# Optimization experiments

Measured on AMD Instinct MI355X. Metric: run time of the kernel, lower is better.

Reference implementation:

```python
import jax, jax.numpy as jnp
import numpy as np

# SPU activation from the RAI-2021 project: x^2 - 0.5 for x>=0, sigmoid(-x)-1 for x<0.

def spu(x):
    s = jax.nn.sigmoid(-x)
    return jnp.where(x >= 0, x * x - 0.5, s - 1.0)

def dspu(x):
    s = jax.nn.sigmoid(-x)
    return jnp.where(x >= 0, 2.0 * x, -s * (1.0 - s))

def get_homog(w, b):
    # [[w, b], [0, 1]]: maps coeff rows over layer outputs (out+1) -> coeffs over inputs (in+1)
    top = jnp.concatenate([w, b[:, None]], axis=1)
    bot = jnp.concatenate([jnp.zeros((1, w.shape[1]), w.dtype), jnp.ones((1, 1), w.dtype)], axis=1)
    return jnp.concatenate([top, bot], axis=0)

def slope_clip(l, u, w_l, w_u):
    # clip slopes into the range spanned by SPU derivatives at the interval endpoints
    k1, k2 = dspu(l), dspu(u)
    klo, khi = jnp.minimum(k1, k2), jnp.maximum(k1, k2)
    return jnp.clip(w_l, klo, khi), jnp.clip(w_u, klo, khi)

def lb_slope(l, u, w_l, w_u):
    # intercepts so that w*x+b lower/upper bounds SPU at the probe points {l, u, mid, 0}
    pts = jnp.stack([l, u, 0.5 * (l + u), jnp.clip(0.0, l, u)], axis=0)  # [4, n]
    b_l = jnp.min(spu(pts) - w_l[None, :] * pts, axis=0)
    b_u = jnp.max(spu(pts) - w_u[None, :] * pts, axis=0)
    return b_l, b_u

def back_sub(Wl, Wu, affine):
    # vectorized back-substitution: the per-row torch.where matmul collapses to
    # relu(l)@W_l + min(l,0)@W_u (and symmetrically for u)
    l, u = Wl[-1], Wu[-1]
    for i in range(len(Wl) - 2, -1, -1):
        if affine[i]:
            l = l @ Wl[i]
            u = u @ Wl[i]
        else:
            l = jnp.maximum(l, 0.0) @ Wl[i] + jnp.minimum(l, 0.0) @ Wu[i]
            u = jnp.maximum(u, 0.0) @ Wu[i] + jnp.minimum(u, 0.0) @ Wl[i]
    return l, u

def _forward(W1, b1, W2, b2, W3, b3, W4, b4, l_in, u_in,
             p_l1, p_u1, p_l2, p_u2, p_l3, p_u3, true_label):
    dt = W1.dtype
    Ws = [get_homog(W1, b1), get_homog(W2, b2), get_homog(W3, b3), get_homog(W4, b4)]
    one = jnp.ones((1, 1), dt)
    l0 = jnp.concatenate([l_in, one], axis=0)  # [d_in+1, 1]
    u0 = jnp.concatenate([u_in, one], axis=0)
    K = Ws[-1].shape[0]  # n_out + 1
    eye = jnp.eye(K, dtype=dt)
    w_out = jnp.concatenate([eye[:true_label], eye[true_label + 1:-1]], axis=0)  # [n_out-1, n_out+1]
    w_out = w_out.at[:, true_label].add(-1.0)
    spu_params = [(p_l1, p_u1), (p_l2, p_u2), (p_l3, p_u3)]
    Wl, Wu, affine = [l0], [u0], [False]
    for i in range(len(Ws)):
        Wl.append(Ws[i]); Wu.append(Ws[i]); affine.append(True)
        if i < len(Ws) - 1:
            l, u = back_sub(Wl, Wu, affine)
            lf, uf = l[:-1, 0], u[:-1, 0]
            pl, pu = spu_params[i]
            cl, cu = slope_clip(lf, uf, pl, pu)
            # torch copies clipped values into the leaf params under no_grad -> straight-through
            wl = pl + jax.lax.stop_gradient(cl - pl)
            wu = pu + jax.lax.stop_gradient(cu - pu)
            b_l, b_u = lb_slope(lf, uf, wl, wu)
            Wl.append(get_homog(jnp.diag(wl), b_l))
            Wu.append(get_homog(jnp.diag(wu), b_u))
            affine.append(False)
    Wl.append(w_out); Wu.append(w_out); affine.append(True)
    _, u = back_sub(Wl, Wu, affine)
    return u.flatten()

def setup_inputs() -> dict:
    key = jax.random.key(0)
    ks = jax.random.split(key, 10)
    d_in, h, n_out = 784, 2048, 10
    s = 0.03
    W1 = jax.random.normal(ks[0], (h, d_in), jnp.float32) * s
    b1 = jax.random.normal(ks[1], (h,), jnp.float32) * s
    W2 = jax.random.normal(ks[2], (h, h), jnp.float32) * s
    b2 = jax.random.normal(ks[3], (h,), jnp.float32) * s
    W3 = jax.random.normal(ks[4], (h, h), jnp.float32) * s
    b3 = jax.random.normal(ks[5], (h,), jnp.float32) * s
    W4 = jax.random.normal(ks[6], (n_out, h), jnp.float32) * s
    b4 = jax.random.normal(ks[7], (n_out,), jnp.float32) * s
    x = jax.random.normal(ks[8], (d_in, 1), jnp.float32)
    eps = 0.05
    return {
        'W1': W1, 'b1': b1, 'W2': W2, 'b2': b2, 'W3': W3, 'b3': b3, 'W4': W4, 'b4': b4,
        'l_in': x - eps, 'u_in': x + eps,
        'p_l1': jnp.zeros((h,), jnp.float32), 'p_u1': jnp.zeros((h,), jnp.float32),
        'p_l2': jnp.zeros((h,), jnp.float32), 'p_u2': jnp.zeros((h,), jnp.float32),
        'p_l3': jnp.zeros((h,), jnp.float32), 'p_u3': jnp.zeros((h,), jnp.float32),
        'true_label': 3,
    }

def reference(W1, b1, W2, b2, W3, b3, W4, b4, l_in, u_in,
              p_l1, p_u1, p_l2, p_u2, p_l3, p_u3, true_label):
    return _forward(W1, b1, W2, b2, W3, b3, W4, b4, l_in, u_in,
                    p_l1, p_u1, p_l2, p_u2, p_l3, p_u3, int(true_label))
```

## Files before the change

### kernel.cpp

```cpp
#include <hip/hip_runtime.h>
#include <math.h>

#define H 2048
#define DIN 784
#define DPAD 896

typedef unsigned short ushort_t;
typedef __attribute__((ext_vector_type(8))) short bf16x8;
typedef __attribute__((ext_vector_type(4))) float f32x4;
typedef __attribute__((ext_vector_type(4))) unsigned short u16x4;
union F4 { float4 v; float a[4]; };
union U4 { u16x4 v; ushort_t a[4]; };

__device__ __forceinline__ float spu_f(float x){
    if (x >= 0.0f) return x*x - 0.5f;
    float s = 1.0f / (1.0f + __expf(x));
    return s - 1.0f;
}
__device__ __forceinline__ float dspu_f(float x){
    if (x >= 0.0f) return 2.0f*x;
    float s = 1.0f / (1.0f + __expf(x));
    return -s * (1.0f - s);
}
__device__ __forceinline__ ushort_t f2bf(float x){
    unsigned u = __float_as_uint(x);
    unsigned r = (u + 0x7FFFu + ((u >> 16) & 1u)) >> 16;
    return (ushort_t)r;
}
__device__ __forceinline__ float bf2f(ushort_t h){
    return __uint_as_float((unsigned)h << 16);
}
__device__ __forceinline__ void load_lds16(const void* g, void* l){
    __builtin_amdgcn_global_load_lds((const __attribute__((address_space(1))) void*)g,
                                     (__attribute__((address_space(3))) void*)l,
                                     16, 0, 0);
}
__device__ __forceinline__ float block_reduce_256(float v, float* red){
    #pragma unroll
    for (int off = 32; off > 0; off >>= 1) v += __shfl_down(v, off, 64);
    int lane = threadIdx.x & 63, w = threadIdx.x >> 6;
    if (lane == 0) red[w] = v;
    __syncthreads();
    float t = 0.f;
    if (threadIdx.x == 0) t = red[0] + red[1] + red[2] + red[3];
    return t;
}
__device__ __forceinline__ void block_reduce2_256(float vl, float vu, float* red,
                                                  float& out_l, float& out_u){
    #pragma unroll
    for (int off = 32; off > 0; off >>= 1){
        vl += __shfl_down(vl, off, 64);
        vu += __shfl_down(vu, off, 64);
    }
    int lane = threadIdx.x & 63, w = threadIdx.x >> 6;
    if (lane == 0){ red[w] = vl; red[4 + w] = vu; }
    __syncthreads();
    if (threadIdx.x == 0){
        out_l = red[0] + red[1] + red[2] + red[3];
        out_u = red[4] + red[5] + red[6] + red[7];
    }
}
__device__ __forceinline__ void spu_relax(float l, float u, float pl, float pu,
                                          float& wl_o, float& wu_o, float& bl_o, float& bu_o){
    float k1 = dspu_f(l), k2 = dspu_f(u);
    float klo = fminf(k1, k2), khi = fmaxf(k1, k2);
    float cwl = fminf(fmaxf(pl, klo), khi);
    float cwu = fminf(fmaxf(pu, klo), khi);
    float pts[4];
    pts[0] = l; pts[1] = u; pts[2] = 0.5f*(l+u); pts[3] = fminf(fmaxf(0.f, l), u);
    float bmin = INFINITY, bmax = -INFINITY;
    #pragma unroll
    for (int t = 0; t < 4; t++){
        float sp = spu_f(pts[t]);
        bmin = fminf(bmin, sp - cwl * pts[t]);
        bmax = fmaxf(bmax, sp - cwu * pts[t]);
    }
    wl_o = cwl; wu_o = cwu; bl_o = bmin; bu_o = bmax;
}

__global__ __launch_bounds__(256) void conv_bounds1(
    const float* __restrict__ W2, ushort_t* __restrict__ T2,
    const float* __restrict__ W1, ushort_t* __restrict__ T1,
    const float* __restrict__ b1,
    const float* __restrict__ l_in, const float* __restrict__ u_in,
    const float* __restrict__ pl, const float* __restrict__ pu,
    float* __restrict__ wl, float* __restrict__ wu,
    float* __restrict__ bl, float* __restrict__ bu)
{
    int z = blockIdx.z;
    if (z < 2){
        __shared__ float tile[32][33];
        const float* W = z ? W1 : W2;
        ushort_t* T = z ? T1 : T2;
        int K = H, N = z ? DIN : H, Npad = z ? DPAD : H;
        if (blockIdx.x * 32 >= (unsigned)Npad) return;
        int n0 = blockIdx.x * 32, k0 = blockIdx.y * 32;
        int tx = threadIdx.x & 31;
        int ty = threadIdx.x >> 5;
        #pragma unroll
        for (int i = 0; i < 32; i += 8){
            int k = k0 + ty + i, n = n0 + tx;
            tile[ty + i][tx] = (k < K && n < N) ? W[(size_t)k * N + n] : 0.f;
        }
        __syncthreads();
        #pragma unroll
        for (int i = 0; i < 32; i += 8){
            int n = n0 + ty + i, k = k0 + tx;
            if (n < Npad && k < K) T[(size_t)n * K + k] = f2bf(tile[tx][ty + i]);
        }
        return;
    }
    int row = blockIdx.y * 64 + blockIdx.x;
    if (row >= H) return;
    __shared__ float red[8];
    const F4* Mr = (const F4*)(W1 + (size_t)row * DIN);
    const F4* li4 = (const F4*)l_in;
    const F4* ui4 = (const F4*)u_in;
    float accl = 0.f, accu = 0.f;
    for (int q = threadIdx.x; q < DIN/4; q += 256){
        F4 v = Mr[q], lo = li4[q], up = ui4[q];
        #pragma unroll
        for (int c = 0; c < 4; c++){
            float p = fmaxf(v.a[c], 0.f), n = fminf(v.a[c], 0.f);
            accl += p * lo.a[c] + n * up.a[c];
            accu += p * up.a[c] + n * lo.a[c];
        }
    }
    float tl, tu;
    block_reduce2_256(accl, accu, red, tl, tu);
    if (threadIdx.x == 0){
        float bb = b1[row];
        spu_relax(tl + bb, tu + bb, pl[row], pu[row],
                  wl[row], wu[row], bl[row], bu[row]);
    }
}

__global__ __launch_bounds__(256) void spu_relax_rows(
    const float* __restrict__ accl, const float* __restrict__ accu,
    const float* __restrict__ c1l, const float* __restrict__ c1u,
    const float* __restrict__ c2l, const float* __restrict__ c2u,
    const float* __restrict__ pl, const float* __restrict__ pu,
    float* __restrict__ wl, float* __restrict__ wu,
    float* __restrict__ bl, float* __restrict__ bu, int n)
{
    int i = blockIdx.x * 256 + threadIdx.x;
    if (i >= n) return;
    float l = accl[i] + c1l[i] + (c2l ? c2l[i] : 0.f);
    float u = accu[i] + c1u[i] + (c2u ? c2u[i] : 0.f);
    spu_relax(l, u, pl[i], pu[i], wl[i], wu[i], bl[i], bu[i]);
}

__global__ __launch_bounds__(256) void dapply_dual(
    const float* __restrict__ S, const float* __restrict__ c_in,
    const float* __restrict__ wl, const float* __restrict__ wu,
    const float* __restrict__ bl, const float* __restrict__ bu,
    const float* __restrict__ bias_next,
    ushort_t* __restrict__ Ml, ushort_t* __restrict__ Mu,
    float* __restrict__ cl_out, float* __restrict__ cu_out, int ncols)
{
    __shared__ float red[8];
    int row = blockIdx.x;
    const F4* S4 = (const F4*)(S + (size_t)row * ncols);
    u16x4* Ml4 = (u16x4*)(Ml + (size_t)row * ncols);
    u16x4* Mu4 = (u16x4*)(Mu + (size_t)row * ncols);
    const F4* wl4 = (const F4*)wl; const F4* wu4 = (const F4*)wu;
    const F4* bl4 = (const F4*)bl; const F4* bu4 = (const F4*)bu;
    const F4* bn4 = (const F4*)bias_next;
    float accl = 0.f, accu = 0.f;
    for (int q = threadIdx.x; q < ncols/4; q += 256){
        F4 v = S4[q], a = wl4[q], b = wu4[q], c = bl4[q], d = bu4[q], e = bn4[q];
        U4 rl, ru;
        #pragma unroll
        for (int k = 0; k < 4; k++){
            float p = fmaxf(v.a[k], 0.f), n = fminf(v.a[k], 0.f);
            float ml = p * a.a[k] + n * b.a[k];
            float mu = p * b.a[k] + n * a.a[k];
            rl.a[k] = f2bf(ml);
            ru.a[k] = f2bf(mu);
            accl += p * c.a[k] + n * d.a[k] + ml * e.a[k];
            accu += p * d.a[k] + n * c.a[k] + mu * e.a[k];
        }
        Ml4[q] = rl.v;
        Mu4[q] = ru.v;
    }
    float tl, tu;
    block_reduce2_256(accl, accu, red, tl, tu);
    if (threadIdx.x == 0){
        float cc = c_in[row];
        cl_out[row] = cc + tl;
        cu_out[row] = cc + tu;
    }
}

__global__ __launch_bounds__(256) void input_reduce(
    const float* __restrict__ M, const float* __restrict__ c,
    const float* __restrict__ pos_b, const float* __restrict__ neg_b,
    float* __restrict__ out, int ncols, int ld)
{
    __shared__ float red[4];
    int row = blockIdx.x;
    const float* Mr = M + (size_t)row * ld;
    float acc = 0.f;
    for (int j = threadIdx.x; j < ncols; j += 256){
        float v = Mr[j];
        acc += fmaxf(v, 0.f) * pos_b[j] + fminf(v, 0.f) * neg_b[j];
    }
    float t = block_reduce_256(acc, red);
    if (threadIdx.x == 0) out[row] = t + c[row];
}

#define TM 128
#define TN 128
#define TK 64
__global__ __launch_bounds__(512, 4) void gemm_nn_fused(
    const ushort_t* __restrict__ A_l, const ushort_t* __restrict__ A_u,
    const ushort_t* __restrict__ BT,
    ushort_t* __restrict__ O_l, ushort_t* __restrict__ O_u,
    const float* __restrict__ wl1, const float* __restrict__ wu1,
    const float* __restrict__ bl1, const float* __restrict__ bu1,
    const float* __restrict__ b1,
    float* __restrict__ cacc_l, float* __restrict__ cacc_u,
    int M, int N, int K)
{
    __shared__ ushort_t As[TM * TK];
    __shared__ ushort_t Bs[TN * TK];
    int lu = blockIdx.z;
    const ushort_t* A = lu ? A_u : A_l;
    ushort_t* O = lu ? O_u : O_l;
    float* cacc = lu ? cacc_u : cacc_l;
    const float* wp_a = lu ? wu1 : wl1;
    const float* wn_a = lu ? wl1 : wu1;
    const float* bp_a = lu ? bu1 : bl1;
    const float* bn_a = lu ? bl1 : bu1;

    int tid  = threadIdx.x;
    int wave = tid >> 6, lane = tid & 63;
    int wm = (wave >> 2) * 64, wn = (wave & 3) * 32;
    int l16 = lane & 15, quad = lane >> 4;
    int row0 = blockIdx.y * TM, col0 = blockIdx.x * TN;

    int r_lo = tid >> 3;
    int kp = (((tid & 7) ^ (r_lo & 7)) * 8);
    const ushort_t *aSrc[2], *bSrc[2];
    ushort_t *aDst[2], *bDst[2];
    #pragma unroll
    for (int g = 0; g < 2; g++){
        aSrc[g] = A  + (size_t)(row0 + g*64 + r_lo) * K + kp;
        bSrc[g] = BT + (size_t)(col0 + g*64 + r_lo) * K + kp;
        aDst[g] = As + g*4096 + wave*512;
        bDst[g] = Bs + g*4096 + wave*512;
    }

    f32x4 acc[4][2];
    #pragma unroll
    for (int i = 0; i < 4; i++)
        #pragma unroll
        for (int j = 0; j < 2; j++)
            acc[i][j] = (f32x4){0.f, 0.f, 0.f, 0.f};

    for (int kk0 = 0; kk0 < K; kk0 += TK){
        #pragma unroll
        for (int g = 0; g < 2; g++) load_lds16(aSrc[g], aDst[g]);
        #pragma unroll
        for (int g = 0; g < 2; g++) load_lds16(bSrc[g], bDst[g]);
        #pragma unroll
        for (int g = 0; g < 2; g++){ aSrc[g] += TK; bSrc[g] += TK; }
        __syncthreads();

        #pragma unroll
        for (int half = 0; half < 2; half++){
            bf16x8 af[4], bf[2];
            #pragma unroll
            for (int t = 0; t < 4; t++){
                int ra = wm + t*16 + l16;
                int sa = (half*4 + quad) ^ (ra & 7);
                af[t] = *(const bf16x8*)&As[ra * TK + sa * 8];
            }
            #pragma unroll
            for (int t = 0; t < 2; t++){
                int rb = wn + t*16 + l16;
                int sb = (half*4 + quad) ^ (rb & 7);
                bf[t] = *(const bf16x8*)&Bs[rb * TK + sb * 8];
            }
            #pragma unroll
            for (int i = 0; i < 4; i++)
                #pragma unroll
                for (int j = 0; j < 2; j++)
                    acc[i][j] = __builtin_amdgcn_mfma_f32_16x16x32_bf16(af[i], bf[j], acc[i][j], 0, 0, 0);
        }
        __syncthreads();
    }

    int cc0 = col0 + wn + l16;
    int cc1 = cc0 + 16;
    float wp0 = wp_a[cc0], wn0 = wn_a[cc0], bp0 = bp_a[cc0], bn0 = bn_a[cc0], bb0 = b1[cc0];
    float wp1 = wp_a[cc1], wn1 = wn_a[cc1], bp1 = bp_a[cc1], bn1 = bn_a[cc1], bb1 = b1[cc1];
    #pragma unroll
    for (int i = 0; i < 4; i++){
        int rbase = row0 + wm + i*16 + quad*4;
        #pragma unroll
        for (int rr = 0; rr < 4; rr++){
            int r = rbase + rr;
            float v0 = acc[i][0][rr];
            float p0 = fmaxf(v0, 0.f), n0 = fminf(v0, 0.f);
            float m0 = p0 * wp0 + n0 * wn0;
            O[(size_t)r * N + cc0] = f2bf(m0);
            float s = p0 * bp0 + n0 * bn0 + m0 * bb0;
            float v1 = acc[i][1][rr];
            float p1 = fmaxf(v1, 0.f), n1 = fminf(v1, 0.f);
            float m1 = p1 * wp1 + n1 * wn1;
            O[(size_t)r * N + cc1] = f2bf(m1);
            s += p1 * bp1 + n1 * bn1 + m1 * bb1;
            s += __shfl_down(s, 8, 16);
            s += __shfl_down(s, 4, 16);
            s += __shfl_down(s, 2, 16);
            s += __shfl_down(s, 1, 16);
            if (l16 == 0) atomicAdd(&cacc[r], s);
        }
    }
}

#define TM2 128
#define TN2 64
__global__ __launch_bounds__(256, 4) void gemm_nd_fused(
    const ushort_t* __restrict__ A_l, const ushort_t* __restrict__ A_u,
    const ushort_t* __restrict__ BT,
    const float* __restrict__ l_in, const float* __restrict__ u_in,
    float* __restrict__ acc_l, float* __restrict__ acc_u,
    int M, int N, int K)
{
    __shared__ ushort_t As[TM2 * TK];
    __shared__ ushort_t Bs[TN2 * TK];
    int lu = blockIdx.z;
    const ushort_t* A = lu ? A_u : A_l;
    float* accv = lu ? acc_u : acc_l;

    int tid  = threadIdx.x;
    int wave = tid >> 6, lane = tid & 63;
    int wm = (wave >> 1) * 64, wn = (wave & 1) * 32;
    int l16 = lane & 15, quad = lane >> 4;
    int row0 = blockIdx.y * TM2, col0 = blockIdx.x * TN2;

    int r_lo = tid >> 3;
    int kp = (((tid & 7) ^ (r_lo & 7)) * 8);
    const ushort_t *aSrc[4], *bSrc[2];
    ushort_t *aDst[4], *bDst[2];
    #pragma unroll
    for (int g = 0; g < 4; g++){
        aSrc[g] = A + (size_t)(row0 + g*32 + r_lo) * K + kp;
        aDst[g] = As + g*2048 + wave*512;
    }
    #pragma unroll
    for (int g = 0; g < 2; g++){
        bSrc[g] = BT + (size_t)(col0 + g*32 + r_lo) * K + kp;
        bDst[g] = Bs + g*2048 + wave*512;
    }

    f32x4 acc[4][2];
    #pragma unroll
    for (int i = 0; i < 4; i++)
        #pragma unroll
        for (int j = 0; j < 2; j++)
            acc[i][j] = (f32x4){0.f, 0.f, 0.f, 0.f};

    for (int kk0 = 0; kk0 < K; kk0 += TK){
        #pragma unroll
        for (int g = 0; g < 4; g++) load_lds16(aSrc[g], aDst[g]);
        #pragma unroll
        for (int g = 0; g < 2; g++) load_lds16(bSrc[g], bDst[g]);
        #pragma unroll
        for (int g = 0; g < 4; g++) aSrc[g] += TK;
        #pragma unroll
        for (int g = 0; g < 2; g++) bSrc[g] += TK;
        __syncthreads();

        #pragma unroll
        for (int half = 0; half < 2; half++){
            bf16x8 af[4], bf[2];
            #pragma unroll
            for (int t = 0; t < 4; t++){
                int ra = wm + t*16 + l16;
                int sa = (half*4 + quad) ^ (ra & 7);
                af[t] = *(const bf16x8*)&As[ra * TK + sa * 8];
            }
            #pragma unroll
            for (int t = 0; t < 2; t++){
                int rb = wn + t*16 + l16;
                int sb = (half*4 + quad) ^ (rb & 7);
                bf[t] = *(const bf16x8*)&Bs[rb * TK + sb * 8];
            }
            #pragma unroll
            for (int i = 0; i < 4; i++)
                #pragma unroll
                for (int j = 0; j < 2; j++)
                    acc[i][j] = __builtin_amdgcn_mfma_f32_16x16x32_bf16(af[i], bf[j], acc[i][j], 0, 0, 0);
        }
        __syncthreads();
    }

    int cc0 = col0 + wn + l16;
    int cc1 = cc0 + 16;
    float pb0 = 0.f, nb0 = 0.f, pb1 = 0.f, nb1 = 0.f;
    if (cc0 < DIN){ pb0 = lu ? u_in[cc0] : l_in[cc0]; nb0 = lu ? l_in[cc0] : u_in[cc0]; }
    if (cc1 < DIN){ pb1 = lu ? u_in[cc1] : l_in[cc1]; nb1 = lu ? l_in[cc1] : u_in[cc1]; }
    #pragma unroll
    for (int i = 0; i < 4; i++){
        int rbase = row0 + wm + i*16 + quad*4;
        #pragma unroll
        for (int rr = 0; rr < 4; rr++){
            int r = rbase + rr;
            float v0 = acc[i][0][rr];
            float s = fmaxf(v0, 0.f) * pb0 + fminf(v0, 0.f) * nb0;
            float v1 = acc[i][1][rr];
            s += fmaxf(v1, 0.f) * pb1 + fminf(v1, 0.f) * nb1;
            s += __shfl_down(s, 8, 16);
            s += __shfl_down(s, 4, 16);
            s += __shfl_down(s, 2, 16);
            s += __shfl_down(s, 1, 16);
            if (l16 == 0) atomicAdd(&accv[r], s);
        }
    }
}

#define GCOLS 64
#define GKS 32
__global__ __launch_bounds__(64) void gemv9_fused(
    const float* __restrict__ S,
    const float* __restrict__ W4, const float* __restrict__ b4,
    const int* __restrict__ tlp, int mode_w4,
    const float* __restrict__ c_in,
    const float* __restrict__ w_pos, const float* __restrict__ w_neg,
    const float* __restrict__ b_pos, const float* __restrict__ b_neg,
    const float* __restrict__ bias_next,
    const float* __restrict__ B, int K, int N,
    float* __restrict__ C, float* __restrict__ c_out)
{
    __shared__ float Alds[9][GKS];
    int j = threadIdx.x;
    int k0 = blockIdx.y * GKS;
    int tl = mode_w4 ? *tlp : 0;
    float pc[9];
    #pragma unroll
    for (int r = 0; r < 9; r++) pc[r] = 0.f;
    if (j < GKS){
        int k = k0 + j;
        float wp = w_pos[k], wn = w_neg[k], bp = b_pos[k], bn = b_neg[k], bb = bias_next[k];
        #pragma unroll
        for (int r = 0; r < 9; r++){
            float v;
            if (mode_w4){
                int kr = r + (r >= tl ? 1 : 0);
                v = W4[(size_t)kr * K + k] - W4[(size_t)tl * K + k];
            } else {
                v = S[(size_t)r * K + k];
            }
            float p = fmaxf(v, 0.f), n = fminf(v, 0.f);
            float m = p * wp + n * wn;
            Alds[r][j] = m;
            pc[r] = p * bp + n * bn + m * bb;
        }
    }
    if (blockIdx.x == 0){
        #pragma unroll
        for (int r = 0; r < 9; r++){
            float v = pc[r];
            #pragma unroll
            for (int o = 32; o > 0; o >>= 1) v += __shfl_down(v, o, 64);
            if (j == 0){
                if (blockIdx.y == 0)
                    v += mode_w4 ? (b4[r + (r >= tl ? 1 : 0)] - b4[tl]) : c_in[r];
                atomicAdd(&c_out[r], v);
            }
        }
    }
    __syncthreads();
    int col = blockIdx.x * GCOLS + j;
    if (col < N){
        float acc[9] = {0.f,0.f,0.f,0.f,0.f,0.f,0.f,0.f,0.f};
        for (int kk = 0; kk < GKS; kk++){
            float b = B[(size_t)(k0 + kk) * N + col];
            #pragma unroll
            for (int r = 0; r < 9; r++) acc[r] += Alds[r][kk] * b;
        }
        #pragma unroll
        for (int r = 0; r < 9; r++) atomicAdd(&C[(size_t)r * N + col], acc[r]);
    }
}

extern "C" void kernel_launch(void* const* d_in, const int* in_sizes, int n_in,
                              void* d_out, int out_size, void* d_ws, size_t ws_size,
                              hipStream_t stream)
{
    const float* W1  = (const float*)d_in[0];
    const float* b1  = (const float*)d_in[1];
    const float* W2  = (const float*)d_in[2];
    const float* b2  = (const float*)d_in[3];
    const float* W3  = (const float*)d_in[4];
    const float* b3  = (const float*)d_in[5];
    const float* W4  = (const float*)d_in[6];
    const float* b4  = (const float*)d_in[7];
    const float* l_in = (const float*)d_in[8];
    const float* u_in = (const float*)d_in[9];
    const float* p_l1 = (const float*)d_in[10];
    const float* p_u1 = (const float*)d_in[11];
    const float* p_l2 = (const float*)d_in[12];
    const float* p_u2 = (const float*)d_in[13];
    const float* p_l3 = (const float*)d_in[14];
    const float* p_u3 = (const float*)d_in[15];
    const int*   tl   = (const int*)d_in[16];
    float* out = (float*)d_out;

    size_t off = 0;
    auto allocB = [&](size_t bytes) -> void* {
        void* p = (char*)d_ws + off;
        off += (bytes + 255) & ~(size_t)255;
        return p;
    };
    ushort_t* W1bt  = (ushort_t*)allocB((size_t)DPAD * H * 2);
    ushort_t* W2bt  = (ushort_t*)allocB((size_t)H * H * 2);
    ushort_t* Abf_l = (ushort_t*)allocB((size_t)H * H * 2);
    ushort_t* Abf_u = (ushort_t*)allocB((size_t)H * H * 2);
    ushort_t* P_l = (ushort_t*)allocB((size_t)H * H * 2);
    ushort_t* P_u = (ushort_t*)allocB((size_t)H * H * 2);
    float *wl1=(float*)allocB(H*4), *wu1=(float*)allocB(H*4), *bl1=(float*)allocB(H*4), *bu1=(float*)allocB(H*4);
    float *wl2=(float*)allocB(H*4), *wu2=(float*)allocB(H*4), *bl2=(float*)allocB(H*4), *bu2=(float*)allocB(H*4);
    float *wl3=(float*)allocB(H*4), *wu3=(float*)allocB(H*4), *bl3=(float*)allocB(H*4), *bu3=(float*)allocB(H*4);
    float *cl_a=(float*)allocB(H*4), *cu_a=(float*)allocB(H*4);
    size_t zero_begin = off;
    float *la2=(float*)allocB(H*4), *ua2=(float*)allocB(H*4);
    float *la3=(float*)allocB(H*4), *ua3=(float*)allocB(H*4);
    float *cl_b=(float*)allocB(H*4), *cu_b=(float*)allocB(H*4);
    float* F1  = (float*)allocB(9 * H * 4);
    float* F2  = (float*)allocB(9 * H * 4);
    float* F3  = (float*)allocB(9 * DIN * 4);
    float *c9b=(float*)allocB(64), *c9c=(float*)allocB(64), *c9d=(float*)allocB(64);
    size_t zero_bytes = off - zero_begin;

    dim3 blk(256);
    dim3 gblk(512);
    dim3 gND(DPAD/TN2, H/TM2, 2);

    hipMemsetAsync((char*)d_ws + zero_begin, 0, zero_bytes, stream);

    conv_bounds1<<<dim3(H/32, H/32, 3), blk, 0, stream>>>(
        W2, W2bt, W1, W1bt, b1, l_in, u_in, p_l1, p_u1, wl1, wu1, bl1, bu1);

    dapply_dual<<<H, blk, 0, stream>>>(W2, b2, wl1, wu1, bl1, bu1, b1,
                                       Abf_l, Abf_u, cl_a, cu_a, H);
    gemm_nd_fused<<<gND, blk, 0, stream>>>(Abf_l, Abf_u, W1bt, l_in, u_in,
                                           la2, ua2, H, DPAD, H);
    spu_relax_rows<<<H/256, blk, 0, stream>>>(la2, ua2, cl_a, cu_a, nullptr, nullptr,
                                              p_l2, p_u2, wl2, wu2, bl2, bu2, H);

    dapply_dual<<<H, blk, 0, stream>>>(W3, b3, wl2, wu2, bl2, bu2, b2,
                                       Abf_l, Abf_u, cl_a, cu_a, H);
    gemm_nn_fused<<<dim3(H/TN, H/TM, 2), gblk, 0, stream>>>(
        Abf_l, Abf_u, W2bt, P_l, P_u,
        wl1, wu1, bl1, bu1, b1, cl_b, cu_b, H, H, H);
    gemm_nd_fused<<<gND, blk, 0, stream>>>(P_l, P_u, W1bt, l_in, u_in,
                                           la3, ua3, H, DPAD, H);
    spu_relax_rows<<<H/256, blk, 0, stream>>>(la3, ua3, cl_b, cu_b, cl_a, cu_a,
                                              p_l3, p_u3, wl3, wu3, bl3, bu3, H);

    gemv9_fused<<<dim3(H/GCOLS, H/GKS), dim3(64), 0, stream>>>(
        nullptr, W4, b4, tl, 1, nullptr,
        wu3, wl3, bu3, bl3, b3, W3, H, H, F1, c9b);
    gemv9_fused<<<dim3(H/GCOLS, H/GKS), dim3(64), 0, stream>>>(
        F1, nullptr, nullptr, nullptr, 0, c9b,
        wu2, wl2, bu2, bl2, b2, W2, H, H, F2, c9c);
    gemv9_fused<<<dim3((DIN + GCOLS - 1)/GCOLS, H/GKS), dim3(64), 0, stream>>>(
        F2, nullptr, nullptr, nullptr, 0, c9c,
        wu1, wl1, bu1, bl1, b1, W1, H, DIN, F3, c9d);
    input_reduce<<<9, blk, 0, stream>>>(F3, c9d, u_in, l_in, out, DIN, DIN);
}
```

Baseline: 313.4 us.

## Fuse SPU relaxation into ND GEMM epilogue via per-row completion counters

Removes the separate spu_relax_rows kernel by having the last contributing block for each row, detected with an atomic counter, compute the SPU relaxation inside the gemm_nd_fused epilogue. The M tile also shrinks from 128 to 64 rows, which doubles the grid and halves per-wave accumulators. This saves two kernel launches but adds a counter atomic and threadfences per row per block. The extra blocks reload the B tiles more often.

New measurement: 1.182 ms. +277.1%, slower.

```diff
diff --git a/kernel.cpp b/kernel.cpp
--- a/kernel.cpp
+++ b/kernel.cpp
@@ -133,21 +133,6 @@
         spu_relax(tl + bb, tu + bb, pl[row], pu[row],
                   wl[row], wu[row], bl[row], bu[row]);
     }
-}
-
-__global__ __launch_bounds__(256) void spu_relax_rows(
-    const float* __restrict__ accl, const float* __restrict__ accu,
-    const float* __restrict__ c1l, const float* __restrict__ c1u,
-    const float* __restrict__ c2l, const float* __restrict__ c2u,
-    const float* __restrict__ pl, const float* __restrict__ pu,
-    float* __restrict__ wl, float* __restrict__ wu,
-    float* __restrict__ bl, float* __restrict__ bu, int n)
-{
-    int i = blockIdx.x * 256 + threadIdx.x;
-    if (i >= n) return;
-    float l = accl[i] + c1l[i] + (c2l ? c2l[i] : 0.f);
-    float u = accu[i] + c1u[i] + (c2u ? c2u[i] : 0.f);
-    spu_relax(l, u, pl[i], pu[i], wl[i], wu[i], bl[i], bu[i]);
 }
 
 __global__ __launch_bounds__(256) void dapply_dual(
@@ -320,77 +305,74 @@
     }
 }
 
-#define TM2 128
 #define TN2 64
 __global__ __launch_bounds__(256, 4) void gemm_nd_fused(
     const ushort_t* __restrict__ A_l, const ushort_t* __restrict__ A_u,
     const ushort_t* __restrict__ BT,
     const float* __restrict__ l_in, const float* __restrict__ u_in,
     float* __restrict__ acc_l, float* __restrict__ acc_u,
-    int M, int N, int K)
-{
-    __shared__ ushort_t As[TM2 * TK];
-    __shared__ ushort_t Bs[TN2 * TK];
+    unsigned* __restrict__ cnt,
+    const float* __restrict__ c1l, const float* __restrict__ c1u,
+    const float* __restrict__ c2l, const float* __restrict__ c2u,
+    const float* __restrict__ pl, const float* __restrict__ pu,
+    float* __restrict__ wl_o, float* __restrict__ wu_o,
+    float* __restrict__ bl_o, float* __restrict__ bu_o,
+    int M, int N, int K, unsigned target)
+{
+    __shared__ ushort_t As[64 * TK];
+    __shared__ ushort_t Bs[64 * TK];
     int lu = blockIdx.z;
     const ushort_t* A = lu ? A_u : A_l;
     float* accv = lu ? acc_u : acc_l;
 
     int tid  = threadIdx.x;
     int wave = tid >> 6, lane = tid & 63;
-    int wm = (wave >> 1) * 64, wn = (wave & 1) * 32;
+    int wm = (wave >> 1) * 32, wn = (wave & 1) * 32;
     int l16 = lane & 15, quad = lane >> 4;
-    int row0 = blockIdx.y * TM2, col0 = blockIdx.x * TN2;
+    int row0 = blockIdx.y * 64, col0 = blockIdx.x * TN2;
 
     int r_lo = tid >> 3;
     int kp = (((tid & 7) ^ (r_lo & 7)) * 8);
-    const ushort_t *aSrc[4], *bSrc[2];
-    ushort_t *aDst[4], *bDst[2];
-    #pragma unroll
-    for (int g = 0; g < 4; g++){
-        aSrc[g] = A + (size_t)(row0 + g*32 + r_lo) * K + kp;
+    const ushort_t *aSrc[2], *bSrc[2];
+    ushort_t *aDst[2], *bDst[2];
+    #pragma unroll
+    for (int g = 0; g < 2; g++){
+        aSrc[g] = A  + (size_t)(row0 + g*32 + r_lo) * K + kp;
+        bSrc[g] = BT + (size_t)(col0 + g*32 + r_lo) * K + kp;
         aDst[g] = As + g*2048 + wave*512;
-    }
-    #pragma unroll
-    for (int g = 0; g < 2; g++){
-        bSrc[g] = BT + (size_t)(col0 + g*32 + r_lo) * K + kp;
         bDst[g] = Bs + g*2048 + wave*512;
     }
 
-    f32x4 acc[4][2];
-    #pragma unroll
-    for (int i = 0; i < 4; i++)
+    f32x4 acc[2][2];
+    #pragma unroll
+    for (int i = 0; i < 2; i++)
         #pragma unroll
         for (int j = 0; j < 2; j++)
             acc[i][j] = (f32x4){0.f, 0.f, 0.f, 0.f};
 
     for (int kk0 = 0; kk0 < K; kk0 += TK){
         #pragma unroll
-        for (int g = 0; g < 4; g++) load_lds16(aSrc[g], aDst[g]);
+        for (int g = 0; g < 2; g++) load_lds16(aSrc[g], aDst[g]);
         #pragma unroll
         for (int g = 0; g < 2; g++) load_lds16(bSrc[g], bDst[g]);
         #pragma unroll
-        for (int g = 0; g < 4; g++) aSrc[g] += TK;
-        #pragma unroll
-        for (int g = 0; g < 2; g++) bSrc[g] += TK;
+        for (int g = 0; g < 2; g++){ aSrc[g] += TK; bSrc[g] += TK; }
         __syncthreads();
 
         #pragma unroll
         for (int half = 0; half < 2; half++){
-            bf16x8 af[4], bf[2];
-            #pragma unroll
-            for (int t = 0; t < 4; t++){
+            bf16x8 af[2], bf[2];
+            #pragma unroll
+            for (int t = 0; t < 2; t++){
                 int ra = wm + t*16 + l16;
                 int sa = (half*4 + quad) ^ (ra & 7);
                 af[t] = *(const bf16x8*)&As[ra * TK + sa * 8];
-            }
-            #pragma unroll
-            for (int t = 0; t < 2; t++){
                 int rb = wn + t*16 + l16;
                 int sb = (half*4 + quad) ^ (rb & 7);
                 bf[t] = *(const bf16x8*)&Bs[rb * TK + sb * 8];
             }
             #pragma unroll
-            for (int i = 0; i < 4; i++)
+            for (int i = 0; i < 2; i++)
                 #pragma unroll
                 for (int j = 0; j < 2; j++)
                     acc[i][j] = __builtin_amdgcn_mfma_f32_16x16x32_bf16(af[i], bf[j], acc[i][j], 0, 0, 0);
@@ -404,7 +386,7 @@
     if (cc0 < DIN){ pb0 = lu ? u_in[cc0] : l_in[cc0]; nb0 = lu ? l_in[cc0] : u_in[cc0]; }
     if (cc1 < DIN){ pb1 = lu ? u_in[cc1] : l_in[cc1]; nb1 = lu ? l_in[cc1] : u_in[cc1]; }
     #pragma unroll
-    for (int i = 0; i < 4; i++){
+    for (int i = 0; i < 2; i++){
         int rbase = row0 + wm + i*16 + quad*4;
         #pragma unroll
         for (int rr = 0; rr < 4; rr++){
@@ -417,7 +399,20 @@
             s += __shfl_down(s, 4, 16);
             s += __shfl_down(s, 2, 16);
             s += __shfl_down(s, 1, 16);
-            if (l16 == 0) atomicAdd(&accv[r], s);
+            if (l16 == 0){
+                atomicAdd(&accv[r], s);
+                __threadfence();
+                unsigned old = atomicAdd(&cnt[r], 1u);
+                if (old == target - 1){
+                    __threadfence();
+                    float lsum = atomicAdd(&acc_l[r], 0.f);
+                    float usum = atomicAdd(&acc_u[r], 0.f);
+                    float lb = lsum + c1l[r] + (c2l ? c2l[r] : 0.f);
+                    float ub = usum + c1u[r] + (c2u ? c2u[r] : 0.f);
+                    spu_relax(lb, ub, pl[r], pu[r],
+                              wl_o[r], wu_o[r], bl_o[r], bu_o[r]);
+                }
+            }
         }
     }
 }
@@ -530,6 +525,7 @@
     float *la2=(float*)allocB(H*4), *ua2=(float*)allocB(H*4);
     float *la3=(float*)allocB(H*4), *ua3=(float*)allocB(H*4);
     float *cl_b=(float*)allocB(H*4), *cu_b=(float*)allocB(H*4);
+    unsigned *cnt2=(unsigned*)allocB(H*4), *cnt3=(unsigned*)allocB(H*4);
     float* F1  = (float*)allocB(9 * H * 4);
     float* F2  = (float*)allocB(9 * H * 4);
     float* F3  = (float*)allocB(9 * DIN * 4);
@@ -538,7 +534,8 @@
 
     dim3 blk(256);
     dim3 gblk(512);
-    dim3 gND(DPAD/TN2, H/TM2, 2);
+    dim3 gND(DPAD/TN2, H/64, 2);
+    const unsigned ND_TARGET = (DPAD/TN2) * 2 * 2;
 
     hipMemsetAsync((char*)d_ws + zero_begin, 0, zero_bytes, stream);
 
@@ -548,9 +545,9 @@
     dapply_dual<<<H, blk, 0, stream>>>(W2, b2, wl1, wu1, bl1, bu1, b1,
                                        Abf_l, Abf_u, cl_a, cu_a, H);
     gemm_nd_fused<<<gND, blk, 0, stream>>>(Abf_l, Abf_u, W1bt, l_in, u_in,
-                                           la2, ua2, H, DPAD, H);
-    spu_relax_rows<<<H/256, blk, 0, stream>>>(la2, ua2, cl_a, cu_a, nullptr, nullptr,
-                                              p_l2, p_u2, wl2, wu2, bl2, bu2, H);
+                                           la2, ua2, cnt2, cl_a, cu_a, nullptr, nullptr,
+                                           p_l2, p_u2, wl2, wu2, bl2, bu2,
+                                           H, DPAD, H, ND_TARGET);
 
     dapply_dual<<<H, blk, 0, stream>>>(W3, b3, wl2, wu2, bl2, bu2, b2,
                                        Abf_l, Abf_u, cl_a, cu_a, H);
@@ -558,9 +555,9 @@
         Abf_l, Abf_u, W2bt, P_l, P_u,
         wl1, wu1, bl1, bu1, b1, cl_b, cu_b, H, H, H);
     gemm_nd_fused<<<gND, blk, 0, stream>>>(P_l, P_u, W1bt, l_in, u_in,
-                                           la3, ua3, H, DPAD, H);
-    spu_relax_rows<<<H/256, blk, 0, stream>>>(la3, ua3, cl_b, cu_b, cl_a, cu_a,
-                                              p_l3, p_u3, wl3, wu3, bl3, bu3, H);
+                                           la3, ua3, cnt3, cl_b, cu_b, cl_a, cu_a,
+                                           p_l3, p_u3, wl3, wu3, bl3, bu3,
+                                           H, DPAD, H, ND_TARGET);
 
     gemv9_fused<<<dim3(H/GCOLS, H/GKS), dim3(64), 0, stream>>>(
         nullptr, W4, b4, tl, 1, nullptr,
```
